# Kernel tuning notes

Measured on AMD Instinct MI355X. Metric: run time of the kernel, lower is better.

Reference implementation:

```python
import jax, jax.numpy as jnp
import numpy as np

SCALE_FACTOR = 2  # init kwarg
KERNEL = 1        # kernel=1 -> no Gaussian inpainting of empty cells
EPS = 1e-6


def token2map_agg(x, loc_orig, idx_agg, H, W):
    """Scatter-average aggregated tokens onto a dense [B,C,H,W] map.

    Faithful to token2map_agg_sparse with weight=None, kernel=1:
      each original position i gets feature x[idx_agg[i]] with weight 1,
      scattered to the grid cell of loc_orig[i]; per-cell average with
      denominator (count + 1e-6).
    """
    B, N, C = x.shape
    N0 = loc_orig.shape[1]
    lo = jnp.clip(loc_orig, -1.0, 1.0)
    wh = jnp.array([W, H], dtype=lo.dtype)
    # normalized [-1,1] -> pixel coords, round-half-even like torch.round
    px = jnp.round(0.5 * (lo + 1.0) * wh - 0.5).astype(jnp.int32)
    ix = jnp.clip(px[..., 0], 0, W - 1)
    iy = jnp.clip(px[..., 1], 0, H - 1)
    seg = (iy * W + ix + jnp.arange(B, dtype=jnp.int32)[:, None] * (H * W)).reshape(-1)  # [B*N0]
    # gather token feature for each original position: [B, N0, C]
    feats = jnp.take_along_axis(x, idx_agg[..., None].astype(jnp.int32), axis=1)
    # scatter features and counts together in one segment_sum
    src = jnp.concatenate([feats, jnp.ones_like(feats[..., :1])], axis=-1).reshape(B * N0, C + 1)
    agg = jax.ops.segment_sum(src, seg, num_segments=B * H * W)  # [B*H*W, C+1]
    out = agg[:, :C] / (agg[:, C:] + EPS)
    return out.reshape(B, H, W, C).transpose(0, 3, 1, 2)  # [B,C,H,W]


def setup_inputs() -> dict:
    key = jax.random.key(0)
    k1, k2, k3, k4 = jax.random.split(key, 4)
    B, N, C = 8, 1024, 128
    N0 = 16384  # 128*128 original grid positions
    x = jax.random.normal(k1, (B, N, C), dtype=jnp.float32)
    loc = jax.random.uniform(k2, (B, N, 2), dtype=jnp.float32, minval=-1.0, maxval=1.0)
    loc_orig = jax.random.uniform(k3, (B, N0, 2), dtype=jnp.float32, minval=-1.0, maxval=1.0)
    idx_agg = jax.random.randint(k4, (B, N0), 0, N, dtype=jnp.int32)
    return {"x": x, "loc": loc, "loc_orig": loc_orig, "idx_agg": idx_agg,
            "map_h": 128, "map_w": 128}


def reference(x, loc, loc_orig, idx_agg, map_h, map_w):
    B, N, C = x.shape
    N0 = idx_agg.shape[1]
    scale_orig = (N0 // N) ** 0.5  # static python value
    if SCALE_FACTOR <= scale_orig:
        h, w = int(map_h * SCALE_FACTOR), int(map_w * SCALE_FACTOR)
        out = token2map_agg(x, loc_orig, idx_agg, h, w)
    else:
        h, w = int(map_h * scale_orig), int(map_w * scale_orig)
        out = token2map_agg(x, loc_orig, idx_agg, h, w)
        h, w = int(map_h * SCALE_FACTOR), int(map_w * SCALE_FACTOR)
        out = jax.image.resize(out, (B, C, h, w), method="bilinear")
    return out
```

## Files before the change

### kernel.cpp

```cpp
#include <hip/hip_runtime.h>

constexpr int B  = 8;
constexpr int N  = 1024;
constexpr int C  = 128;
constexpr int N0 = 16384;
constexpr int HH = 256;
constexpr int WW = 256;
constexpr int HW = HH * WW;
constexpr int NPTS = B * N0;
constexpr int NCELL = B * HW;

constexpr int CPG    = 256;
constexpr int GPB    = HW / CPG;
constexpr int NGRP   = B * GPB;
constexpr int CSPLIT = 4;
constexpr int CHB    = C / CSPLIT;
constexpr int CAP    = 192;

constexpr int ROWW = CPG + 4;
constexpr int ACC_WORDS = CHB * ROWW;

typedef float vfloat4 __attribute__((ext_vector_type(4)));

__device__ __forceinline__ int cell_of(float lx, float ly) {
    lx = fminf(fmaxf(lx, -1.0f), 1.0f);
    ly = fminf(fmaxf(ly, -1.0f), 1.0f);
    float pxf = rintf(0.5f * (lx + 1.0f) * 256.0f - 0.5f);
    float pyf = rintf(0.5f * (ly + 1.0f) * 256.0f - 0.5f);
    int ix = (int)pxf; ix = ix < 0 ? 0 : (ix > WW - 1 ? WW - 1 : ix);
    int iy = (int)pyf; iy = iy < 0 ? 0 : (iy > HH - 1 ? HH - 1 : iy);
    return iy * WW + ix;
}

__global__ void bucket_kernel(const float* __restrict__ loc_orig,
                              const int* __restrict__ idx_agg,
                              int* __restrict__ cursor,
                              int* __restrict__ cellcnt,
                              int* __restrict__ bucket) {
    int t = blockIdx.x * blockDim.x + threadIdx.x;
    int p0 = t * 2;
    if (p0 >= NPTS) return;
    float4 l2 = ((const float4*)loc_orig)[t];
    int2  ia  = ((const int2*)idx_agg)[t];
    int b = p0 >> 14;
    #pragma unroll
    for (int k = 0; k < 2; ++k) {
        float lx = k ? l2.z : l2.x;
        float ly = k ? l2.w : l2.y;
        int tok  = k ? ia.y : ia.x;
        int cell = cell_of(lx, ly);
        int gcell = b * HW + cell;
        atomicAdd(cellcnt + gcell, 1);
        int g = b * GPB + (cell >> 8);
        int pos = atomicAdd(cursor + g, 1);
        if (pos < CAP)
            __builtin_nontemporal_store(((cell & 255) << 10) | tok,
                                        bucket + g * CAP + pos);
    }
}

__global__ __launch_bounds__(512) void gather_kernel(
        const float* __restrict__ x,
        const int* __restrict__ cursor,
        const int* __restrict__ cellcnt,
        const int* __restrict__ bucket,
        float* __restrict__ out) {
    __shared__ __align__(16) float acc[ACC_WORDS];
    __shared__ int recs[CAP];
    __shared__ int cnt_s;

    int gid    = blockIdx.x;
    int bgrp   = gid & (NGRP - 1);
    int csplit = gid >> 11;
    int b      = bgrp >> 8;
    int cell0  = (bgrp & 255) * CPG;
    int ch0    = csplit * CHB;
    int tid    = threadIdx.x;
    int wave   = tid >> 6, lane = tid & 63;

    int my_cnt = (tid == 0) ? cursor[bgrp] : 0;
    int my_rec = (tid < CAP) ? bucket[bgrp * CAP + tid] : 0;

    float4 z4 = make_float4(0.f, 0.f, 0.f, 0.f);
    for (int i = tid; i < ACC_WORDS / 4; i += 512) ((float4*)acc)[i] = z4;
    if (tid == 0) cnt_s = my_cnt > CAP ? CAP : my_cnt;
    if (tid < CAP) recs[tid] = my_rec;
    __syncthreads();

    int cnt = cnt_s;
    int chl = lane & 15;
    const float* xb = x + (size_t)b * N * C + ch0;
    for (int base = wave * 4; base < cnt; base += 32) {
        int p = base + (lane >> 4);
        if (p < cnt) {
            int e = recs[p];
            int local = e >> 10;
            int tok   = e & 1023;
            float2 v = ((const float2*)(xb + (size_t)tok * C))[chl];
            atomicAdd(&acc[chl * ROWW + local],        v.x);
            atomicAdd(&acc[(chl + 16) * ROWW + local], v.y);
        }
    }
    __syncthreads();

    int q  = tid & 63;
    int i4 = q * 4;
    int cl = tid >> 6;
    int4 c4 = *(const int4*)(cellcnt + b * HW + cell0 + i4);
    float4 s;
    s.x = 1.0f / ((float)c4.x + 1e-6f);
    s.y = 1.0f / ((float)c4.y + 1e-6f);
    s.z = 1.0f / ((float)c4.z + 1e-6f);
    s.w = 1.0f / ((float)c4.w + 1e-6f);
    float* obase = out + (size_t)b * C * HW + cell0;
    #pragma unroll
    for (int it = 0; it < 4; ++it) {
        int c  = it * 8 + cl;
        int rr = (c >> 1) + ((c & 1) << 4);
        float4 v = *(const float4*)&acc[rr * ROWW + i4];
        vfloat4 nv = { v.x * s.x, v.y * s.y, v.z * s.z, v.w * s.w };
        __builtin_nontemporal_store(nv,
            (vfloat4*)(obase + (size_t)(ch0 + c) * HW + i4));
    }
}

extern "C" void kernel_launch(void* const* d_in, const int* in_sizes, int n_in,
                              void* d_out, int out_size, void* d_ws, size_t ws_size,
                              hipStream_t stream) {
    const float* x        = (const float*)d_in[0];
    const float* loc_orig = (const float*)d_in[2];
    const int*   idx_agg  = (const int*)d_in[3];
    float* out = (float*)d_out;

    int* cursor  = (int*)d_ws;
    int* cellcnt = cursor + NGRP;
    int* bucket  = cellcnt + NCELL;

    (void)hipMemsetAsync(cursor, 0, (NGRP + NCELL) * sizeof(int), stream);
    bucket_kernel<<<(NPTS / 2 + 255) / 256, 256, 0, stream>>>(loc_orig, idx_agg,
                                                              cursor, cellcnt, bucket);
    gather_kernel<<<NGRP * CSPLIT, 512, 0, stream>>>(x, cursor, cellcnt, bucket, out);
}
```

Measured before the change: 348.2 us.

## Restructure gather into per-channel slab blocks with LDS-cached token column

Bucketing now groups points into 8 large slabs per batch instead of 256-cell groups. The cursor counters are padded 64 ints apart to avoid contention between neighbouring atomics. The gather launches one block per (batch, channel, slab). Each block caches that channel's 1024-token column in shared memory, scatter-adds all slab records into an 8192-cell shared accumulator, and writes a contiguous normalized output row. The intent is fully coalesced, long output writes and fewer global gathers per record. The cost is that each block does 1024 strided loads of x, and the bucket records are re-read once per channel; the nontemporal output stores are also dropped.

```diff
diff --git a/kernel.cpp b/kernel.cpp
--- a/kernel.cpp
+++ b/kernel.cpp
@@ -10,17 +10,11 @@
 constexpr int NPTS = B * N0;
 constexpr int NCELL = B * HW;
 
-constexpr int CPG    = 256;
-constexpr int GPB    = HW / CPG;
-constexpr int NGRP   = B * GPB;
-constexpr int CSPLIT = 4;
-constexpr int CHB    = C / CSPLIT;
-constexpr int CAP    = 192;
-
-constexpr int ROWW = CPG + 4;
-constexpr int ACC_WORDS = CHB * ROWW;
-
-typedef float vfloat4 __attribute__((ext_vector_type(4)));
+constexpr int SLABS      = 8;
+constexpr int SLAB_CELLS = HW / SLABS;
+constexpr int NGRP       = B * SLABS;
+constexpr int CAPR       = 2560;
+constexpr int CURSTRIDE  = 64;
 
 __device__ __forceinline__ int cell_of(float lx, float ly) {
     lx = fminf(fmaxf(lx, -1.0f), 1.0f);
@@ -49,13 +43,10 @@
         float ly = k ? l2.w : l2.y;
         int tok  = k ? ia.y : ia.x;
         int cell = cell_of(lx, ly);
-        int gcell = b * HW + cell;
-        atomicAdd(cellcnt + gcell, 1);
-        int g = b * GPB + (cell >> 8);
-        int pos = atomicAdd(cursor + g, 1);
-        if (pos < CAP)
-            __builtin_nontemporal_store(((cell & 255) << 10) | tok,
-                                        bucket + g * CAP + pos);
+        atomicAdd(cellcnt + b * HW + cell, 1);
+        int g = b * SLABS + (cell >> 13);
+        int pos = atomicAdd(cursor + g * CURSTRIDE, 1);
+        if (pos < CAPR) bucket[g * CAPR + pos] = ((cell & 8191) << 10) | tok;
     }
 }
 
@@ -65,62 +56,48 @@
         const int* __restrict__ cellcnt,
         const int* __restrict__ bucket,
         float* __restrict__ out) {
-    __shared__ __align__(16) float acc[ACC_WORDS];
-    __shared__ int recs[CAP];
-    __shared__ int cnt_s;
+    __shared__ __align__(16) float acc[SLAB_CELLS];
+    __shared__ float xc[N];
 
-    int gid    = blockIdx.x;
-    int bgrp   = gid & (NGRP - 1);
-    int csplit = gid >> 11;
-    int b      = bgrp >> 8;
-    int cell0  = (bgrp & 255) * CPG;
-    int ch0    = csplit * CHB;
-    int tid    = threadIdx.x;
-    int wave   = tid >> 6, lane = tid & 63;
+    int gid  = blockIdx.x;
+    int slab = gid & (SLABS - 1);
+    int bc   = gid >> 3;
+    int c    = bc & (C - 1);
+    int b    = bc >> 7;
+    int g    = b * SLABS + slab;
+    int tid  = threadIdx.x;
 
-    int my_cnt = (tid == 0) ? cursor[bgrp] : 0;
-    int my_rec = (tid < CAP) ? bucket[bgrp * CAP + tid] : 0;
+    const float* xb = x + ((size_t)b * N) * C + c;
+    float v0 = xb[(size_t)tid * C];
+    float v1 = xb[(size_t)(tid + 512) * C];
+    int cnt = cursor[g * CURSTRIDE];
+    cnt = cnt > CAPR ? CAPR : cnt;
 
     float4 z4 = make_float4(0.f, 0.f, 0.f, 0.f);
-    for (int i = tid; i < ACC_WORDS / 4; i += 512) ((float4*)acc)[i] = z4;
-    if (tid == 0) cnt_s = my_cnt > CAP ? CAP : my_cnt;
-    if (tid < CAP) recs[tid] = my_rec;
+    for (int i = tid; i < SLAB_CELLS / 4; i += 512) ((float4*)acc)[i] = z4;
+    xc[tid]       = v0;
+    xc[tid + 512] = v1;
     __syncthreads();
 
-    int cnt = cnt_s;
-    int chl = lane & 15;
-    const float* xb = x + (size_t)b * N * C + ch0;
-    for (int base = wave * 4; base < cnt; base += 32) {
-        int p = base + (lane >> 4);
-        if (p < cnt) {
-            int e = recs[p];
-            int local = e >> 10;
-            int tok   = e & 1023;
-            float2 v = ((const float2*)(xb + (size_t)tok * C))[chl];
-            atomicAdd(&acc[chl * ROWW + local],        v.x);
-            atomicAdd(&acc[(chl + 16) * ROWW + local], v.y);
-        }
+    const int* recs = bucket + g * CAPR;
+    for (int i = tid; i < cnt; i += 512) {
+        int e = recs[i];
+        atomicAdd(&acc[e >> 10], xc[e & 1023]);
     }
     __syncthreads();
 
-    int q  = tid & 63;
-    int i4 = q * 4;
-    int cl = tid >> 6;
-    int4 c4 = *(const int4*)(cellcnt + b * HW + cell0 + i4);
-    float4 s;
-    s.x = 1.0f / ((float)c4.x + 1e-6f);
-    s.y = 1.0f / ((float)c4.y + 1e-6f);
-    s.z = 1.0f / ((float)c4.z + 1e-6f);
-    s.w = 1.0f / ((float)c4.w + 1e-6f);
-    float* obase = out + (size_t)b * C * HW + cell0;
+    const int* cc = cellcnt + b * HW + slab * SLAB_CELLS;
+    float* ob = out + ((size_t)(b * C + c)) * HW + slab * SLAB_CELLS;
     #pragma unroll
     for (int it = 0; it < 4; ++it) {
-        int c  = it * 8 + cl;
-        int rr = (c >> 1) + ((c & 1) << 4);
-        float4 v = *(const float4*)&acc[rr * ROWW + i4];
-        vfloat4 nv = { v.x * s.x, v.y * s.y, v.z * s.z, v.w * s.w };
-        __builtin_nontemporal_store(nv,
-            (vfloat4*)(obase + (size_t)(ch0 + c) * HW + i4));
+        int i = it * 512 + tid;
+        int4 c4 = ((const int4*)cc)[i];
+        float4 a = ((const float4*)acc)[i];
+        a.x *= 1.0f / ((float)c4.x + 1e-6f);
+        a.y *= 1.0f / ((float)c4.y + 1e-6f);
+        a.z *= 1.0f / ((float)c4.z + 1e-6f);
+        a.w *= 1.0f / ((float)c4.w + 1e-6f);
+        ((float4*)ob)[i] = a;
     }
 }
 
@@ -133,11 +110,11 @@
     float* out = (float*)d_out;
 
     int* cursor  = (int*)d_ws;
-    int* cellcnt = cursor + NGRP;
+    int* cellcnt = cursor + NGRP * CURSTRIDE;
     int* bucket  = cellcnt + NCELL;
 
-    (void)hipMemsetAsync(cursor, 0, (NGRP + NCELL) * sizeof(int), stream);
+    (void)hipMemsetAsync(cursor, 0, (NGRP * CURSTRIDE + NCELL) * sizeof(int), stream);
     bucket_kernel<<<(NPTS / 2 + 255) / 256, 256, 0, stream>>>(loc_orig, idx_agg,
                                                               cursor, cellcnt, bucket);
-    gather_kernel<<<NGRP * CSPLIT, 512, 0, stream>>>(x, cursor, cellcnt, bucket, out);
+    gather_kernel<<<B * C * SLABS, 512, 0, stream>>>(x, cursor, cellcnt, bucket, out);
 }
```

Measured after the change: 370.5 us. +6.4%, slower.

## Make gather kernel persistent with double-buffered shared accumulators

Applied to the files above, without the earlier changes.

The gather kernel becomes a persistent grid of 512 blocks that loop over all tiles. Shared accumulator and record buffers are ping-ponged between two copies so one barrier per tile can be dropped. Nontemporal stores for the bucket records and output are replaced with plain stores. The aim is to cut block launch and setup overhead, at the cost of doubled LDS per block, which lowers occupancy, and output writes that may now pollute cache.

```diff
diff --git a/kernel.cpp b/kernel.cpp
--- a/kernel.cpp
+++ b/kernel.cpp
@@ -16,11 +16,11 @@
 constexpr int CSPLIT = 4;
 constexpr int CHB    = C / CSPLIT;
 constexpr int CAP    = 192;
+constexpr int NTILES = NGRP * CSPLIT;
+constexpr int GBLK   = 512;
 
 constexpr int ROWW = CPG + 4;
 constexpr int ACC_WORDS = CHB * ROWW;
-
-typedef float vfloat4 __attribute__((ext_vector_type(4)));
 
 __device__ __forceinline__ int cell_of(float lx, float ly) {
     lx = fminf(fmaxf(lx, -1.0f), 1.0f);
@@ -49,13 +49,10 @@
         float ly = k ? l2.w : l2.y;
         int tok  = k ? ia.y : ia.x;
         int cell = cell_of(lx, ly);
-        int gcell = b * HW + cell;
-        atomicAdd(cellcnt + gcell, 1);
+        atomicAdd(cellcnt + b * HW + cell, 1);
         int g = b * GPB + (cell >> 8);
         int pos = atomicAdd(cursor + g, 1);
-        if (pos < CAP)
-            __builtin_nontemporal_store(((cell & 255) << 10) | tok,
-                                        bucket + g * CAP + pos);
+        if (pos < CAP) bucket[g * CAP + pos] = ((cell & 255) << 10) | tok;
     }
 }
 
@@ -65,62 +62,63 @@
         const int* __restrict__ cellcnt,
         const int* __restrict__ bucket,
         float* __restrict__ out) {
-    __shared__ __align__(16) float acc[ACC_WORDS];
-    __shared__ int recs[CAP];
-    __shared__ int cnt_s;
+    __shared__ __align__(16) float acc[2][ACC_WORDS];
+    __shared__ int recs[2][CAP];
 
-    int gid    = blockIdx.x;
-    int bgrp   = gid & (NGRP - 1);
-    int csplit = gid >> 11;
-    int b      = bgrp >> 8;
-    int cell0  = (bgrp & 255) * CPG;
-    int ch0    = csplit * CHB;
-    int tid    = threadIdx.x;
-    int wave   = tid >> 6, lane = tid & 63;
+    int tid  = threadIdx.x;
+    int wave = tid >> 6, lane = tid & 63;
+    int chl  = lane & 15;
 
-    int my_cnt = (tid == 0) ? cursor[bgrp] : 0;
-    int my_rec = (tid < CAP) ? bucket[bgrp * CAP + tid] : 0;
+    int pp = 0;
+    for (int tile = blockIdx.x; tile < NTILES; tile += GBLK, pp ^= 1) {
+        int bgrp   = tile & (NGRP - 1);
+        int csplit = tile >> 11;
+        int b      = bgrp >> 8;
+        int cell0  = (bgrp & 255) * CPG;
+        int ch0    = csplit * CHB;
 
-    float4 z4 = make_float4(0.f, 0.f, 0.f, 0.f);
-    for (int i = tid; i < ACC_WORDS / 4; i += 512) ((float4*)acc)[i] = z4;
-    if (tid == 0) cnt_s = my_cnt > CAP ? CAP : my_cnt;
-    if (tid < CAP) recs[tid] = my_rec;
-    __syncthreads();
+        int cnt = cursor[bgrp];
+        cnt = cnt > CAP ? CAP : cnt;
+        int my_rec = (tid < CAP) ? bucket[bgrp * CAP + tid] : 0;
 
-    int cnt = cnt_s;
-    int chl = lane & 15;
-    const float* xb = x + (size_t)b * N * C + ch0;
-    for (int base = wave * 4; base < cnt; base += 32) {
-        int p = base + (lane >> 4);
-        if (p < cnt) {
-            int e = recs[p];
-            int local = e >> 10;
-            int tok   = e & 1023;
-            float2 v = ((const float2*)(xb + (size_t)tok * C))[chl];
-            atomicAdd(&acc[chl * ROWW + local],        v.x);
-            atomicAdd(&acc[(chl + 16) * ROWW + local], v.y);
+        float4 z4 = make_float4(0.f, 0.f, 0.f, 0.f);
+        float4* a4 = (float4*)acc[pp];
+        for (int i = tid; i < ACC_WORDS / 4; i += 512) a4[i] = z4;
+        if (tid < CAP) recs[pp][tid] = my_rec;
+        __syncthreads();
+
+        const float* xb = x + (size_t)b * N * C + ch0;
+        for (int base = wave * 4; base < cnt; base += 32) {
+            int p = base + (lane >> 4);
+            if (p < cnt) {
+                int e = recs[pp][p];
+                int local = e >> 10;
+                int tok   = e & 1023;
+                float2 v = ((const float2*)(xb + (size_t)tok * C))[chl];
+                atomicAdd(&acc[pp][chl * ROWW + local],        v.x);
+                atomicAdd(&acc[pp][(chl + 16) * ROWW + local], v.y);
+            }
         }
-    }
-    __syncthreads();
+        __syncthreads();
 
-    int q  = tid & 63;
-    int i4 = q * 4;
-    int cl = tid >> 6;
-    int4 c4 = *(const int4*)(cellcnt + b * HW + cell0 + i4);
-    float4 s;
-    s.x = 1.0f / ((float)c4.x + 1e-6f);
-    s.y = 1.0f / ((float)c4.y + 1e-6f);
-    s.z = 1.0f / ((float)c4.z + 1e-6f);
-    s.w = 1.0f / ((float)c4.w + 1e-6f);
-    float* obase = out + (size_t)b * C * HW + cell0;
-    #pragma unroll
-    for (int it = 0; it < 4; ++it) {
-        int c  = it * 8 + cl;
-        int rr = (c >> 1) + ((c & 1) << 4);
-        float4 v = *(const float4*)&acc[rr * ROWW + i4];
-        vfloat4 nv = { v.x * s.x, v.y * s.y, v.z * s.z, v.w * s.w };
-        __builtin_nontemporal_store(nv,
-            (vfloat4*)(obase + (size_t)(ch0 + c) * HW + i4));
+        int q  = tid & 63;
+        int i4 = q * 4;
+        int cl = tid >> 6;
+        int4 c4 = *(const int4*)(cellcnt + b * HW + cell0 + i4);
+        float4 s;
+        s.x = 1.0f / ((float)c4.x + 1e-6f);
+        s.y = 1.0f / ((float)c4.y + 1e-6f);
+        s.z = 1.0f / ((float)c4.z + 1e-6f);
+        s.w = 1.0f / ((float)c4.w + 1e-6f);
+        float* obase = out + (size_t)b * C * HW + cell0;
+        #pragma unroll
+        for (int it = 0; it < 4; ++it) {
+            int c  = it * 8 + cl;
+            int rr = (c >> 1) + ((c & 1) << 4);
+            float4 v = *(const float4*)&acc[pp][rr * ROWW + i4];
+            v.x *= s.x; v.y *= s.y; v.z *= s.z; v.w *= s.w;
+            *(float4*)(obase + (size_t)(ch0 + c) * HW + i4) = v;
+        }
     }
 }
 
@@ -139,5 +137,5 @@
     (void)hipMemsetAsync(cursor, 0, (NGRP + NCELL) * sizeof(int), stream);
     bucket_kernel<<<(NPTS / 2 + 255) / 256, 256, 0, stream>>>(loc_orig, idx_agg,
                                                               cursor, cellcnt, bucket);
-    gather_kernel<<<NGRP * CSPLIT, 512, 0, stream>>>(x, cursor, cellcnt, bucket, out);
+    gather_kernel<<<GBLK, 512, 0, stream>>>(x, cursor, cellcnt, bucket, out);
 }
```

After: 355.4 us. 2.1% more time.
